# Performance work log

Measured on AMD Instinct MI355X. Metric: run time of the kernel, lower is better.

Reference implementation:

```python
import jax, jax.numpy as jnp
import numpy as np

N_NODES = 100000
N_EDGES = 1600000
VOCAB = 1000
EMB_DIM = 64
OUT_DIM = 32


def setup_inputs() -> dict:
    key = jax.random.key(0)
    k1, k2, k3, k4, k5 = jax.random.split(key, 5)
    node_seq = jax.random.randint(k1, (N_NODES,), 0, VOCAB, dtype=jnp.int64)
    edge_index = jax.random.randint(k2, (2, N_EDGES), 0, N_NODES, dtype=jnp.int64)
    edge_weight = jax.random.uniform(k3, (N_EDGES,), dtype=jnp.float32)
    emb = jax.random.normal(k4, (VOCAB, EMB_DIM), dtype=jnp.float32)
    W = jax.random.normal(k5, (EMB_DIM, OUT_DIM), dtype=jnp.float32) * (1.0 / np.sqrt(EMB_DIM))
    b = jnp.zeros((OUT_DIM,), dtype=jnp.float32)
    return {"node_seq": node_seq, "edge_index": edge_index, "edge_weight": edge_weight,
            "emb": emb, "W": W, "b": b}


def reference(node_seq, edge_index, edge_weight, emb, W, b):
    N = node_seq.shape[0]
    # Embedding lookup: [N, EMB_DIM]
    x = emb[node_seq]
    # Linear transform first (GCNConv applies lin before propagate): [N, OUT_DIM]
    xw = x @ W
    # Add self loops with weight 1 (PyG GCNConv default add_self_loops=True, fill_value=1)
    loop = jnp.arange(N, dtype=edge_index.dtype)
    row = jnp.concatenate([edge_index[0], loop])
    col = jnp.concatenate([edge_index[1], loop])
    w = jnp.concatenate([edge_weight, jnp.ones((N,), dtype=edge_weight.dtype)])
    # Symmetric gcn_norm: deg over targets, norm = d^{-1/2}[row] * w * d^{-1/2}[col]
    deg = jax.ops.segment_sum(w, col, num_segments=N)
    dis = jnp.where(deg > 0, jax.lax.rsqrt(jnp.where(deg > 0, deg, 1.0)), 0.0)
    norm = dis[row] * w * dis[col]
    # Gather messages from source nodes, scale, scatter-add into targets
    msgs = norm[:, None] * xw[row]            # [E+N, OUT_DIM]
    out = jax.ops.segment_sum(msgs, col, num_segments=N) + b  # [N, OUT_DIM]
    # Mean pool over nodes
    return out.mean(axis=0)
```

## Files before the change

kernel.cpp:

```cpp
#include <hip/hip_runtime.h>

#define N_NODES 100000
#define N_EDGES 1600000
#define VOCAB   1000
#define EMB_DIM 64
#define OUT_DIM 32

#define BKT_BITS 9
#define BKT_SIZE 512
#define NBKT ((N_NODES + BKT_SIZE - 1) / BKT_SIZE)
#define CAP  10240
#define NSB  512
#define CHUNK (N_EDGES / NSB)
#define SPLIT 4
#define NPART (NBKT * SPLIT)
#define NRF_BLOCKS 250

__device__ __forceinline__ void fatomic_add(float* p, float v) {
    unsafeAtomicAdd(p, v);
}

__global__ void k_init(int* __restrict__ cursors, int* __restrict__ done) {
    int i = threadIdx.x;
    if (i < NBKT) cursors[i] = 0;
    if (i == NBKT) *done = 0;
}

__global__ void __launch_bounds__(256) k_scatter(
        const int* __restrict__ row, const int* __restrict__ col,
        const float* __restrict__ w, int* __restrict__ cursors,
        uint2* __restrict__ recs) {
    __shared__ uint2 stage[CHUNK];
    __shared__ unsigned char seg[CHUNK];
    __shared__ int cnt[NBKT], lofs[NBKT], gbase[NBKT];
    __shared__ int sc[256];
    const int tid = threadIdx.x;
    const int e0 = blockIdx.x * CHUNK;

    for (int i = tid; i < NBKT; i += 256) cnt[i] = 0;
    __syncthreads();
    for (int i = tid; i < CHUNK; i += 256)
        atomicAdd(&cnt[col[e0 + i] >> BKT_BITS], 1);
    __syncthreads();
    sc[tid] = (tid < NBKT) ? cnt[tid] : 0;
    __syncthreads();
    for (int d = 1; d < 256; d <<= 1) {
        int v = (tid >= d) ? sc[tid - d] : 0;
        __syncthreads();
        sc[tid] += v;
        __syncthreads();
    }
    if (tid < NBKT) {
        lofs[tid]  = sc[tid] - cnt[tid];
        gbase[tid] = tid * CAP + atomicAdd(&cursors[tid], cnt[tid]);
        cnt[tid]   = 0;
    }
    __syncthreads();
    for (int i = tid; i < CHUNK; i += 256) {
        int c = col[e0 + i];
        int r = row[e0 + i];
        int b = c >> BKT_BITS;
        int p = lofs[b] + atomicAdd(&cnt[b], 1);
        stage[p] = make_uint2(((unsigned)r << BKT_BITS) | (unsigned)(c & (BKT_SIZE - 1)),
                              __float_as_uint(w[e0 + i]));
        seg[p] = (unsigned char)b;
    }
    __syncthreads();
    for (int i = tid; i < CHUNK; i += 256) {
        int b = seg[i];
        recs[gbase[b] + (i - lofs[b])] = stage[i];
    }
}

__global__ void __launch_bounds__(512) k_dis(
        const uint2* __restrict__ recs, const int* __restrict__ cursors,
        const int* __restrict__ node_seq, uint2* __restrict__ disseq) {
    __shared__ float acc[BKT_SIZE];
    const int b = blockIdx.x;
    if (threadIdx.x < BKT_SIZE) acc[threadIdx.x] = 0.0f;
    __syncthreads();
    const int base = b * CAP;
    const int cnt = cursors[b];
    for (int i = threadIdx.x; i < cnt; i += 512) {
        uint2 r = recs[base + i];
        fatomic_add(&acc[r.x & (BKT_SIZE - 1)], __uint_as_float(r.y));
    }
    __syncthreads();
    const int n0 = b << BKT_BITS;
    if (threadIdx.x < BKT_SIZE) {
        int n = n0 + threadIdx.x;
        if (n < N_NODES)
            disseq[n] = make_uint2(__float_as_uint(__frsqrt_rn(1.0f + acc[threadIdx.x])),
                                   (unsigned)node_seq[n]);
    }
}

__global__ void __launch_bounds__(512) k_coeff(
        const uint2* __restrict__ recs, const int* __restrict__ cursors,
        const uint2* __restrict__ disseq, float* __restrict__ gcoeff) {
    __shared__ float dloc[BKT_SIZE];
    __shared__ float lc[VOCAB];
    const int b = blockIdx.x >> 2, s = blockIdx.x & 3;
    const int n0 = b << BKT_BITS;
    for (int i = threadIdx.x; i < VOCAB; i += 512) lc[i] = 0.0f;
    if (threadIdx.x < BKT_SIZE) {
        int n = n0 + threadIdx.x;
        dloc[threadIdx.x] = (n < N_NODES) ? __uint_as_float(disseq[n].x) : 0.0f;
    }
    __syncthreads();
    const int base = b * CAP;
    const int cnt = cursors[b];
    const int lo = (cnt * s) >> 2;
    const int hi = (cnt * (s + 1)) >> 2;
    for (int i = lo + threadIdx.x; i < hi; i += 512) {
        uint2 rec = recs[base + i];
        int lcol = rec.x & (BKT_SIZE - 1);
        int r    = rec.x >> BKT_BITS;
        uint2 ds = disseq[r];
        fatomic_add(&lc[ds.y],
            __uint_as_float(ds.x) * __uint_as_float(rec.y) * dloc[lcol]);
    }
    if (s == 0 && threadIdx.x < BKT_SIZE) {
        int n = n0 + threadIdx.x;
        if (n < N_NODES) {
            uint2 ds = disseq[n];
            float d = __uint_as_float(ds.x);
            fatomic_add(&lc[ds.y], d * d);
        }
    }
    __syncthreads();
    for (int i = threadIdx.x; i < VOCAB; i += 512)
        gcoeff[blockIdx.x * VOCAB + i] = lc[i];
}

__global__ void __launch_bounds__(256) k_reduce_final(
        const float* __restrict__ gcoeff, const float* __restrict__ emb,
        const float* __restrict__ W, const float* __restrict__ bias,
        float* __restrict__ tpart, int* __restrict__ done,
        float* __restrict__ out) {
    __shared__ float tk[EMB_DIM];
    __shared__ int lastflag;
    const int tid = threadIdx.x;
    const int l = tid & 63;
    if (tid < EMB_DIM) tk[tid] = 0.0f;
    __syncthreads();
    {
        const int v = (blockIdx.x * 256 + tid) >> 6;
        float s = 0.0f;
        for (int p = l; p < NPART; p += 64) s += gcoeff[p * VOCAB + v];
        for (int off = 32; off > 0; off >>= 1) s += __shfl_down(s, off, 64);
        float cv = __shfl(s, 0, 64);
        fatomic_add(&tk[l], cv * emb[v * EMB_DIM + l]);
    }
    __syncthreads();
    if (tid < EMB_DIM) tpart[blockIdx.x * EMB_DIM + tid] = tk[tid];
    __syncthreads();
    if (tid == 0) {
        __threadfence();
        lastflag = (atomicAdd(done, 1) == NRF_BLOCKS - 1) ? 1 : 0;
    }
    __syncthreads();
    if (lastflag) {
        __threadfence();
        __shared__ float tk2[4][EMB_DIM];
        const int g = tid >> 6;
        float s = 0.0f;
        for (int p = g; p < NRF_BLOCKS; p += 4)
            s += ((volatile float*)tpart)[p * EMB_DIM + l];
        tk2[g][l] = s;
        __syncthreads();
        if (tid < EMB_DIM)
            tk[tid] = tk2[0][tid] + tk2[1][tid] + tk2[2][tid] + tk2[3][tid];
        __syncthreads();
        if (tid < OUT_DIM) {
            float s2 = 0.0f;
            #pragma unroll
            for (int k = 0; k < EMB_DIM; ++k) s2 += tk[k] * W[k * OUT_DIM + tid];
            out[tid] = s2 * (1.0f / (float)N_NODES) + bias[tid];
        }
    }
}

extern "C" void kernel_launch(void* const* d_in, const int* in_sizes, int n_in,
                              void* d_out, int out_size, void* d_ws, size_t ws_size,
                              hipStream_t stream) {
    const int*   node_seq = (const int*)  d_in[0];
    const int*   eidx     = (const int*)  d_in[1];
    const float* ew       = (const float*)d_in[2];
    const float* emb      = (const float*)d_in[3];
    const float* W        = (const float*)d_in[4];
    const float* bias     = (const float*)d_in[5];
    float*       out      = (float*)d_out;

    const int* row = eidx;
    const int* col = eidx + N_EDGES;

    char* wsb = (char*)d_ws;
    const size_t REC_BYTES = (size_t)NBKT * CAP * sizeof(uint2);
    uint2* recs    = (uint2*)wsb;
    int*   cursors = (int*)(wsb + REC_BYTES);
    int*   done    = cursors + NBKT;
    uint2* disseq  = (uint2*)(wsb + REC_BYTES + 4096);
    float* gcoeff  = (float*)(disseq + N_NODES);
    float* tpart   = gcoeff + (size_t)NPART * VOCAB;

    k_init<<<1, 256, 0, stream>>>(cursors, done);
    k_scatter<<<NSB, 256, 0, stream>>>(row, col, ew, cursors, recs);
    k_dis<<<NBKT, 512, 0, stream>>>(recs, cursors, node_seq, disseq);
    k_coeff<<<NPART, 512, 0, stream>>>(recs, cursors, disseq, gcoeff);
    k_reduce_final<<<NRF_BLOCKS, 256, 0, stream>>>(gcoeff, emb, W, bias,
                                                   tpart, done, out);
}
```

Baseline: 158.3 us.

## Use wave-shuffle scan, larger blocks, and drop k_coeff bucket splitting

```diff
diff --git a/kernel.cpp b/kernel.cpp
--- a/kernel.cpp
+++ b/kernel.cpp
@@ -11,9 +11,9 @@
 #define NBKT ((N_NODES + BKT_SIZE - 1) / BKT_SIZE)
 #define CAP  10240
 #define NSB  512
+#define STPB 512
 #define CHUNK (N_EDGES / NSB)
-#define SPLIT 4
-#define NPART (NBKT * SPLIT)
+#define NPART NBKT
 #define NRF_BLOCKS 250
 
 __device__ __forceinline__ void fatomic_add(float* p, float v) {
@@ -26,37 +26,42 @@
     if (i == NBKT) *done = 0;
 }
 
-__global__ void __launch_bounds__(256) k_scatter(
+__global__ void __launch_bounds__(STPB) k_scatter(
         const int* __restrict__ row, const int* __restrict__ col,
         const float* __restrict__ w, int* __restrict__ cursors,
         uint2* __restrict__ recs) {
     __shared__ uint2 stage[CHUNK];
     __shared__ unsigned char seg[CHUNK];
     __shared__ int cnt[NBKT], lofs[NBKT], gbase[NBKT];
-    __shared__ int sc[256];
     const int tid = threadIdx.x;
     const int e0 = blockIdx.x * CHUNK;
 
-    for (int i = tid; i < NBKT; i += 256) cnt[i] = 0;
-    __syncthreads();
-    for (int i = tid; i < CHUNK; i += 256)
+    for (int i = tid; i < NBKT; i += STPB) cnt[i] = 0;
+    __syncthreads();
+    for (int i = tid; i < CHUNK; i += STPB)
         atomicAdd(&cnt[col[e0 + i] >> BKT_BITS], 1);
     __syncthreads();
-    sc[tid] = (tid < NBKT) ? cnt[tid] : 0;
-    __syncthreads();
-    for (int d = 1; d < 256; d <<= 1) {
-        int v = (tid >= d) ? sc[tid - d] : 0;
-        __syncthreads();
-        sc[tid] += v;
-        __syncthreads();
-    }
-    if (tid < NBKT) {
-        lofs[tid]  = sc[tid] - cnt[tid];
-        gbase[tid] = tid * CAP + atomicAdd(&cursors[tid], cnt[tid]);
-        cnt[tid]   = 0;
-    }
-    __syncthreads();
-    for (int i = tid; i < CHUNK; i += 256) {
+    if (tid < 64) {
+        const int b4 = tid * 4;
+        int c0 = (b4 + 0 < NBKT) ? cnt[b4 + 0] : 0;
+        int c1 = (b4 + 1 < NBKT) ? cnt[b4 + 1] : 0;
+        int c2 = (b4 + 2 < NBKT) ? cnt[b4 + 2] : 0;
+        int c3 = (b4 + 3 < NBKT) ? cnt[b4 + 3] : 0;
+        int s0 = c0, s1 = s0 + c1, s2 = s1 + c2, s3 = s2 + c3;
+        int sc = s3;
+        #pragma unroll
+        for (int d = 1; d < 64; d <<= 1) {
+            int o = __shfl_up(sc, d, 64);
+            if (tid >= d) sc += o;
+        }
+        const int excl = sc - s3;
+        if (b4 + 0 < NBKT) { lofs[b4+0] = excl;      gbase[b4+0] = (b4+0)*CAP + atomicAdd(&cursors[b4+0], c0); cnt[b4+0] = 0; }
+        if (b4 + 1 < NBKT) { lofs[b4+1] = excl + s0; gbase[b4+1] = (b4+1)*CAP + atomicAdd(&cursors[b4+1], c1); cnt[b4+1] = 0; }
+        if (b4 + 2 < NBKT) { lofs[b4+2] = excl + s1; gbase[b4+2] = (b4+2)*CAP + atomicAdd(&cursors[b4+2], c2); cnt[b4+2] = 0; }
+        if (b4 + 3 < NBKT) { lofs[b4+3] = excl + s2; gbase[b4+3] = (b4+3)*CAP + atomicAdd(&cursors[b4+3], c3); cnt[b4+3] = 0; }
+    }
+    __syncthreads();
+    for (int i = tid; i < CHUNK; i += STPB) {
         int c = col[e0 + i];
         int r = row[e0 + i];
         int b = c >> BKT_BITS;
@@ -66,13 +71,13 @@
         seg[p] = (unsigned char)b;
     }
     __syncthreads();
-    for (int i = tid; i < CHUNK; i += 256) {
+    for (int i = tid; i < CHUNK; i += STPB) {
         int b = seg[i];
         recs[gbase[b] + (i - lofs[b])] = stage[i];
     }
 }
 
-__global__ void __launch_bounds__(512) k_dis(
+__global__ void __launch_bounds__(1024) k_dis(
         const uint2* __restrict__ recs, const int* __restrict__ cursors,
         const int* __restrict__ node_seq, uint2* __restrict__ disseq) {
     __shared__ float acc[BKT_SIZE];
@@ -81,7 +86,7 @@
     __syncthreads();
     const int base = b * CAP;
     const int cnt = cursors[b];
-    for (int i = threadIdx.x; i < cnt; i += 512) {
+    for (int i = threadIdx.x; i < cnt; i += 1024) {
         uint2 r = recs[base + i];
         fatomic_add(&acc[r.x & (BKT_SIZE - 1)], __uint_as_float(r.y));
     }
@@ -95,14 +100,14 @@
     }
 }
 
-__global__ void __launch_bounds__(512) k_coeff(
+__global__ void __launch_bounds__(1024) k_coeff(
         const uint2* __restrict__ recs, const int* __restrict__ cursors,
         const uint2* __restrict__ disseq, float* __restrict__ gcoeff) {
     __shared__ float dloc[BKT_SIZE];
     __shared__ float lc[VOCAB];
-    const int b = blockIdx.x >> 2, s = blockIdx.x & 3;
+    const int b = blockIdx.x;
     const int n0 = b << BKT_BITS;
-    for (int i = threadIdx.x; i < VOCAB; i += 512) lc[i] = 0.0f;
+    if (threadIdx.x < VOCAB) lc[threadIdx.x] = 0.0f;
     if (threadIdx.x < BKT_SIZE) {
         int n = n0 + threadIdx.x;
         dloc[threadIdx.x] = (n < N_NODES) ? __uint_as_float(disseq[n].x) : 0.0f;
@@ -110,9 +115,7 @@
     __syncthreads();
     const int base = b * CAP;
     const int cnt = cursors[b];
-    const int lo = (cnt * s) >> 2;
-    const int hi = (cnt * (s + 1)) >> 2;
-    for (int i = lo + threadIdx.x; i < hi; i += 512) {
+    for (int i = threadIdx.x; i < cnt; i += 1024) {
         uint2 rec = recs[base + i];
         int lcol = rec.x & (BKT_SIZE - 1);
         int r    = rec.x >> BKT_BITS;
@@ -120,7 +123,7 @@
         fatomic_add(&lc[ds.y],
             __uint_as_float(ds.x) * __uint_as_float(rec.y) * dloc[lcol]);
     }
-    if (s == 0 && threadIdx.x < BKT_SIZE) {
+    if (threadIdx.x < BKT_SIZE) {
         int n = n0 + threadIdx.x;
         if (n < N_NODES) {
             uint2 ds = disseq[n];
@@ -129,8 +132,8 @@
         }
     }
     __syncthreads();
-    for (int i = threadIdx.x; i < VOCAB; i += 512)
-        gcoeff[blockIdx.x * VOCAB + i] = lc[i];
+    if (threadIdx.x < VOCAB)
+        gcoeff[b * VOCAB + threadIdx.x] = lc[threadIdx.x];
 }
 
 __global__ void __launch_bounds__(256) k_reduce_final(
@@ -205,9 +208,9 @@
     float* tpart   = gcoeff + (size_t)NPART * VOCAB;
 
     k_init<<<1, 256, 0, stream>>>(cursors, done);
-    k_scatter<<<NSB, 256, 0, stream>>>(row, col, ew, cursors, recs);
-    k_dis<<<NBKT, 512, 0, stream>>>(recs, cursors, node_seq, disseq);
-    k_coeff<<<NPART, 512, 0, stream>>>(recs, cursors, disseq, gcoeff);
+    k_scatter<<<NSB, STPB, 0, stream>>>(row, col, ew, cursors, recs);
+    k_dis<<<NBKT, 1024, 0, stream>>>(recs, cursors, node_seq, disseq);
+    k_coeff<<<NBKT, 1024, 0, stream>>>(recs, cursors, disseq, gcoeff);
     k_reduce_final<<<NRF_BLOCKS, 256, 0, stream>>>(gcoeff, emb, W, bias,
                                                    tpart, done, out);
 }
```

Result: slower. 175.9 us (+11.2%).
